# Kernel optimization log

Hardware: AMD Instinct MI355X
Metric: run time of the kernel (lower is better)

## Reference

```python
import jax, jax.numpy as jnp
import numpy as np

N = 500_000
N_ATOMS = 5
T = 8                # angle triplets per (residue, bead) table row
CONT_LEN = 36
GATE_OFFSET = 1
NUM_EXPERTS = 18
BEAD_COL = 36
MAX_BEADS = 4
ANGLE_WEIGHT = 1.0
EPS = 1e-8
MIN_LEN = 0.02


def setup_inputs() -> dict:
    key = jax.random.key(0)
    ks = jax.random.split(key, 8)
    x = jax.random.uniform(ks[0], (N, 38), dtype=jnp.float32)
    # gate column holds residue id in [1, num_experts]; bead column in [0, max_beads)
    res = jax.random.randint(ks[1], (N,), 1, NUM_EXPERTS + 1).astype(jnp.float32)
    bead = jax.random.randint(ks[2], (N,), 0, MAX_BEADS).astype(jnp.float32)
    x = x.at[:, CONT_LEN + 1].set(res)
    x = x.at[:, BEAD_COL].set(bead)
    y_true = jax.random.normal(ks[3], (N, N_ATOMS * 3), dtype=jnp.float32)
    y_pred = jax.random.normal(ks[4], (N, N_ATOMS * 3), dtype=jnp.float32)
    mask = (jax.random.uniform(ks[5], (N, N_ATOMS * 3)) < 0.85).astype(jnp.float32)
    # -1 entries act as invalid-triplet sentinels (trip_ok branch)
    trip = jax.random.randint(ks[6], (NUM_EXPERTS, MAX_BEADS, T, 3), -1, N_ATOMS, dtype=jnp.int32)
    valid = jax.random.randint(ks[7], (NUM_EXPERTS, MAX_BEADS, T), 0, 2, dtype=jnp.int32)
    return {"x": x, "y_true": y_true, "y_pred": y_pred, "mask": mask,
            "angle_triplets_table": trip, "angle_valid_table": valid}


def _atom_mse(true, pred, m):
    # masked per-atom squared error, normalized by count of valid atoms per sample
    se_atom = jnp.sum(jnp.square(true - pred) * m, axis=-1)          # [N, A]
    atom_valid = jnp.any(m > 0.0, axis=-1).astype(se_atom.dtype)     # [N, A]
    num = jnp.sum(se_atom * atom_valid, axis=-1)
    den = jnp.sum(atom_valid, axis=-1) + EPS
    return jnp.mean(num / den)


def _angle_loss(x, true, pred, m, trip_table, valid_table):
    gate = x[:, CONT_LEN + 1]
    gate = jnp.where(jnp.isfinite(gate), gate, 0.0)
    res_id = jnp.clip(jnp.round(gate).astype(jnp.int32) - GATE_OFFSET, 0, NUM_EXPERTS - 1)
    bead = x[:, BEAD_COL]
    bead = jnp.where(jnp.isfinite(bead), bead, 0.0)
    bead_id = jnp.clip(jnp.round(bead).astype(jnp.int32), 0, MAX_BEADS - 1)

    atom_valid = jnp.any(m > 0.0, axis=-1)                           # [N, A]
    trip = trip_table[res_id, bead_id]                               # [N, T, 3]
    base_valid = valid_table[res_id, bead_id]                        # [N, T]
    trip_ok = jnp.all(trip >= 0, axis=-1)
    ts = jnp.maximum(trip, 0)
    i_idx, j_idx, k_idx = ts[..., 0], ts[..., 1], ts[..., 2]         # [N, T]

    rows = jnp.arange(true.shape[0])[:, None]
    vi = atom_valid[rows, i_idx]
    vj = atom_valid[rows, j_idx]
    vk = atom_valid[rows, k_idx]
    ti, tj, tk = true[rows, i_idx], true[rows, j_idx], true[rows, k_idx]   # [N, T, 3]
    pi, pj, pk = pred[rows, i_idx], pred[rows, j_idx], pred[rows, k_idx]

    v1t, v2t, v1p, v2p = ti - tj, tk - tj, pi - pj, pk - pj
    ml2 = jnp.float32(MIN_LEN * MIN_LEN)
    sq = lambda v: jnp.sum(jnp.square(v), axis=-1)
    l1t2, l2t2, l1p2, l2p2 = sq(v1t), sq(v2t), sq(v1p), sq(v2p)

    valid = (trip_ok & (base_valid > 0) & vi & vj & vk
             & (l1t2 > ml2) & (l2t2 > ml2) & (l1p2 > ml2) & (l2p2 > ml2))

    unit = lambda v, l2: v * jax.lax.rsqrt(jnp.maximum(l2, ml2))[..., None]
    u1t, u2t = unit(v1t, l1t2), unit(v2t, l2t2)
    u1p, u2p = unit(v1p, l1p2), unit(v2p, l2p2)

    clip = lambda c: jnp.clip(c, -1.0 + 1e-6, 1.0 - 1e-6)
    cos_t = clip(jnp.sum(u1t * u2t, axis=-1))
    cos_p = clip(jnp.sum(u1p * u2p, axis=-1))
    sin_t = jnp.linalg.norm(jnp.cross(u1t, u2t), axis=-1)
    sin_p = jnp.linalg.norm(jnp.cross(u1p, u2p), axis=-1)

    per_ang = jnp.square(cos_p - cos_t) + jnp.square(sin_p - sin_t)
    per_ang = jnp.where(valid, per_ang, 0.0)
    num = jnp.sum(per_ang, axis=-1)
    den = jnp.sum(valid.astype(jnp.float32), axis=-1) + EPS
    return jnp.mean(num / den)


def reference(x, y_true, y_pred, mask, angle_triplets_table, angle_valid_table):
    true = y_true.reshape(-1, N_ATOMS, 3).astype(jnp.float32)
    pred = y_pred.reshape(-1, N_ATOMS, 3).astype(jnp.float32)
    m = mask.reshape(-1, N_ATOMS, 3).astype(jnp.float32)
    atom = _atom_mse(true, pred, m)
    ang = _angle_loss(x, true, pred, m, angle_triplets_table, angle_valid_table)
    return atom + ANGLE_WEIGHT * ang
```

## Files before the change

### kernel.cpp

```cpp
#include <hip/hip_runtime.h>
#include <math.h>

#define NATOMS 5
#define NEXP 18
#define NBEAD 4
#define EPSV 1e-8f
#define ML2 (0.02f * 0.02f)

__global__ void pack_tables(const int* __restrict__ trip, const int* __restrict__ valid,
                            int4* __restrict__ ptbl) {
    int c = blockIdx.x * blockDim.x + threadIdx.x;
    if (c < NEXP * NBEAD) {
        unsigned wv[4] = {0u, 0u, 0u, 0u};
#pragma unroll
        for (int t = 0; t < 8; t++) {
            int b = c * 8 + t;
            int i = trip[b * 3 + 0], j = trip[b * 3 + 1], k = trip[b * 3 + 2];
            int ok = (i >= 0 && j >= 0 && k >= 0 && valid[b] > 0) ? 1 : 0;
            int ic = min(max(i, 0), NATOMS - 1);
            int jc = min(max(j, 0), NATOMS - 1);
            int kc = min(max(k, 0), NATOMS - 1);
            unsigned e = (unsigned)ic | ((unsigned)jc << 3) | ((unsigned)kc << 6) |
                         ((unsigned)ok << 9);
            wv[t >> 1] |= e << ((t & 1) * 16);
        }
        ptbl[c] = make_int4((int)wv[0], (int)wv[1], (int)wv[2], (int)wv[3]);
    }
}

__device__ __forceinline__ void sel5(const float* a, int idx, float& vx, float& vy, float& vz) {
    vx = a[0]; vy = a[1]; vz = a[2];
#pragma unroll
    for (int q = 1; q < 5; q++) {
        bool c = (idx == q);
        vx = c ? a[3 * q + 0] : vx;
        vy = c ? a[3 * q + 1] : vy;
        vz = c ? a[3 * q + 2] : vz;
    }
}

__global__ __launch_bounds__(256) void loss_kernel(
    const float* __restrict__ xin, const float* __restrict__ y_true,
    const float* __restrict__ y_pred, const float* __restrict__ mask,
    const int4* __restrict__ ptbl, float* __restrict__ out, int n, float inv_n) {
    __shared__ float sT[3840];
    __shared__ float sP[3840];
    __shared__ float sM[3840];
    __shared__ float red[4];

    const int row0 = blockIdx.x * 256;
    int rows = n - row0;
    if (rows > 256) rows = 256;
    const int cnt = rows * 15;
    const int cnt4 = cnt >> 2;

    const float4* gt = reinterpret_cast<const float4*>(y_true + (size_t)row0 * 15);
    const float4* gp = reinterpret_cast<const float4*>(y_pred + (size_t)row0 * 15);
    const float4* gm = reinterpret_cast<const float4*>(mask + (size_t)row0 * 15);
    for (int i = threadIdx.x; i < cnt4; i += 256) {
        reinterpret_cast<float4*>(sT)[i] = gt[i];
        reinterpret_cast<float4*>(sP)[i] = gp[i];
        reinterpret_cast<float4*>(sM)[i] = gm[i];
    }
    for (int i = (cnt4 << 2) + threadIdx.x; i < cnt; i += 256) {
        sT[i] = y_true[(size_t)row0 * 15 + i];
        sP[i] = y_pred[(size_t)row0 * 15 + i];
        sM[i] = mask[(size_t)row0 * 15 + i];
    }
    __syncthreads();

    float result = 0.0f;
    const int row = row0 + threadIdx.x;
    if (row < n) {
        float T[15], P[15];
        const float* st = sT + threadIdx.x * 15;
        const float* sp = sP + threadIdx.x * 15;
        const float* sm = sM + threadIdx.x * 15;
#pragma unroll
        for (int c = 0; c < 15; c++) { T[c] = st[c]; P[c] = sp[c]; }

        float num_a = 0.f, den_a = 0.f;
        int avm = 0;
#pragma unroll
        for (int a = 0; a < 5; a++) {
            float se = 0.f;
            bool av = false;
#pragma unroll
            for (int c = 0; c < 3; c++) {
                float m = sm[a * 3 + c];
                float d = T[a * 3 + c] - P[a * 3 + c];
                se = fmaf(d * d, m, se);
                av = av || (m > 0.f);
            }
            if (av) { num_a += se; den_a += 1.f; avm |= (1 << a); }
        }
        result = num_a / (den_a + EPSV);

        float2 gb = *reinterpret_cast<const float2*>(xin + (size_t)row * 38 + 36);
        float bead = gb.x, gate = gb.y;
        if (!isfinite(gate)) gate = 0.f;
        if (!isfinite(bead)) bead = 0.f;
        gate = fminf(fmaxf(gate, -64.f), 64.f);
        bead = fminf(fmaxf(bead, -64.f), 64.f);
        int res_id = min(max((int)rintf(gate) - 1, 0), NEXP - 1);
        int bead_id = min(max((int)rintf(bead), 0), NBEAD - 1);

        int4 pk = ptbl[res_id * NBEAD + bead_id];
        unsigned pw0 = (unsigned)pk.x, pw1 = (unsigned)pk.y;
        unsigned pw2 = (unsigned)pk.z, pw3 = (unsigned)pk.w;

        float num_g = 0.f, den_g = 0.f;
#pragma unroll
        for (int t = 0; t < 8; t++) {
            unsigned wrd = (t < 2) ? pw0 : (t < 4) ? pw1 : (t < 6) ? pw2 : pw3;
            unsigned e = (wrd >> ((t & 1) * 16)) & 0xffffu;
            int ii = e & 7, jj = (e >> 3) & 7, kk = (e >> 6) & 7;
            bool wok = ((e >> 9) & 1u) != 0u;

            float tix, tiy, tiz, tjx, tjy, tjz, tkx, tky, tkz;
            sel5(T, ii, tix, tiy, tiz);
            sel5(T, jj, tjx, tjy, tjz);
            sel5(T, kk, tkx, tky, tkz);
            float pix, piy, piz, pjx, pjy, pjz, pkx, pky, pkz;
            sel5(P, ii, pix, piy, piz);
            sel5(P, jj, pjx, pjy, pjz);
            sel5(P, kk, pkx, pky, pkz);

            float v1tx = tix - tjx, v1ty = tiy - tjy, v1tz = tiz - tjz;
            float v2tx = tkx - tjx, v2ty = tky - tjy, v2tz = tkz - tjz;
            float v1px = pix - pjx, v1py = piy - pjy, v1pz = piz - pjz;
            float v2px = pkx - pjx, v2py = pky - pjy, v2pz = pkz - pjz;

            float l1t = v1tx * v1tx + v1ty * v1ty + v1tz * v1tz;
            float l2t = v2tx * v2tx + v2ty * v2ty + v2tz * v2tz;
            float l1p = v1px * v1px + v1py * v1py + v1pz * v1pz;
            float l2p = v2px * v2px + v2py * v2py + v2pz * v2pz;

            bool valid = wok && ((avm >> ii) & 1) && ((avm >> jj) & 1) && ((avm >> kk) & 1) &&
                         (l1t > ML2) && (l2t > ML2) && (l1p > ML2) && (l2p > ML2);

            float rt = rsqrtf(fmaxf(l1t, ML2)) * rsqrtf(fmaxf(l2t, ML2));
            float rp = rsqrtf(fmaxf(l1p, ML2)) * rsqrtf(fmaxf(l2p, ML2));

            float dott = v1tx * v2tx + v1ty * v2ty + v1tz * v2tz;
            float dotp = v1px * v2px + v1py * v2py + v1pz * v2pz;
            float cost = fminf(fmaxf(dott * rt, -1.f + 1e-6f), 1.f - 1e-6f);
            float cosp = fminf(fmaxf(dotp * rp, -1.f + 1e-6f), 1.f - 1e-6f);

            float cxt = v1ty * v2tz - v1tz * v2ty;
            float cyt = v1tz * v2tx - v1tx * v2tz;
            float czt = v1tx * v2ty - v1ty * v2tx;
            float sint = sqrtf(cxt * cxt + cyt * cyt + czt * czt) * rt;
            float cxp = v1py * v2pz - v1pz * v2py;
            float cyp = v1pz * v2px - v1px * v2pz;
            float czp = v1px * v2py - v1py * v2px;
            float sinp = sqrtf(cxp * cxp + cyp * cyp + czp * czp) * rp;

            float dc = cosp - cost, dsn = sinp - sint;
            float pa = dc * dc + dsn * dsn;
            if (valid) { num_g += pa; den_g += 1.f; }
        }
        result += num_g / (den_g + EPSV);
    }

#pragma unroll
    for (int off = 32; off > 0; off >>= 1)
        result += __shfl_down(result, off, 64);
    int lane = threadIdx.x & 63, wv = threadIdx.x >> 6;
    if (lane == 0) red[wv] = result;
    __syncthreads();
    if (threadIdx.x == 0) {
        float s = red[0] + red[1] + red[2] + red[3];
        atomicAdd(out, s * inv_n);
    }
}

extern "C" void kernel_launch(void* const* d_in, const int* in_sizes, int n_in,
                              void* d_out, int out_size, void* d_ws, size_t ws_size,
                              hipStream_t stream) {
    const float* x = (const float*)d_in[0];
    const float* y_true = (const float*)d_in[1];
    const float* y_pred = (const float*)d_in[2];
    const float* mask = (const float*)d_in[3];
    const int* trip = (const int*)d_in[4];
    const int* valid = (const int*)d_in[5];
    float* out = (float*)d_out;

    const int n = in_sizes[1] / 15;
    int4* ptbl = (int4*)d_ws;

    hipMemsetAsync(out, 0, sizeof(float), stream);
    pack_tables<<<1, 128, 0, stream>>>(trip, valid, ptbl);
    const int blocks = (n + 255) / 256;
    loss_kernel<<<blocks, 256, 0, stream>>>(x, y_true, y_pred, mask, ptbl, out, n,
                                            1.0f / (float)n);
}
```

Before: 198.1 us.

## Fuse table packing into loss kernel, bit-pack mask in LDS, simplify angle math

Drops the separate pack_tables launch: each block now rebuilds the triplet table in shared memory (three 10-bit-packed words per entry) from the global trip/valid arrays. The mask is no longer staged as floats in LDS but compressed into a 15-bit per-row bitmask through shared atomicOr, which cuts LDS footprint. That footprint cut makes the higher occupancy hint in launch_bounds(256,5) feasible. Sine is derived from the cosine as sqrt(1-c^2) instead of cross products, with one combined rsq per vector pair. The trade-offs are redundant table construction in every block, LDS atomics, and slightly different numerics for the sine term.

Result: faster. 193.9 us (-2.1%).

```diff
diff --git a/kernel.cpp b/kernel.cpp
--- a/kernel.cpp
+++ b/kernel.cpp
@@ -7,27 +7,6 @@
 #define EPSV 1e-8f
 #define ML2 (0.02f * 0.02f)
 
-__global__ void pack_tables(const int* __restrict__ trip, const int* __restrict__ valid,
-                            int4* __restrict__ ptbl) {
-    int c = blockIdx.x * blockDim.x + threadIdx.x;
-    if (c < NEXP * NBEAD) {
-        unsigned wv[4] = {0u, 0u, 0u, 0u};
-#pragma unroll
-        for (int t = 0; t < 8; t++) {
-            int b = c * 8 + t;
-            int i = trip[b * 3 + 0], j = trip[b * 3 + 1], k = trip[b * 3 + 2];
-            int ok = (i >= 0 && j >= 0 && k >= 0 && valid[b] > 0) ? 1 : 0;
-            int ic = min(max(i, 0), NATOMS - 1);
-            int jc = min(max(j, 0), NATOMS - 1);
-            int kc = min(max(k, 0), NATOMS - 1);
-            unsigned e = (unsigned)ic | ((unsigned)jc << 3) | ((unsigned)kc << 6) |
-                         ((unsigned)ok << 9);
-            wv[t >> 1] |= e << ((t & 1) * 16);
-        }
-        ptbl[c] = make_int4((int)wv[0], (int)wv[1], (int)wv[2], (int)wv[3]);
-    }
-}
-
 __device__ __forceinline__ void sel5(const float* a, int idx, float& vx, float& vy, float& vz) {
     vx = a[0]; vy = a[1]; vz = a[2];
 #pragma unroll
@@ -39,81 +18,118 @@
     }
 }
 
-__global__ __launch_bounds__(256) void loss_kernel(
+__global__ __launch_bounds__(256, 5) void loss_kernel(
     const float* __restrict__ xin, const float* __restrict__ y_true,
     const float* __restrict__ y_pred, const float* __restrict__ mask,
-    const int4* __restrict__ ptbl, float* __restrict__ out, int n, float inv_n) {
+    const int* __restrict__ trip, const int* __restrict__ valid,
+    float* __restrict__ out, int n, float inv_n) {
     __shared__ float sT[3840];
     __shared__ float sP[3840];
-    __shared__ float sM[3840];
+    __shared__ unsigned sMask[256];
+    __shared__ unsigned sTbl[72][3];
     __shared__ float red[4];
+
+    const int tid = threadIdx.x;
+
+    sMask[tid] = 0u;
+    if (tid < NEXP * NBEAD) {
+        unsigned w0 = 0u, w1 = 0u, w2 = 0u;
+#pragma unroll
+        for (int t = 0; t < 8; t++) {
+            int b = tid * 8 + t;
+            int i = trip[b * 3 + 0], j = trip[b * 3 + 1], k = trip[b * 3 + 2];
+            unsigned ok = (i >= 0 && j >= 0 && k >= 0 && valid[b] > 0) ? 1u : 0u;
+            unsigned ic = (unsigned)min(max(i, 0), NATOMS - 1);
+            unsigned jc = (unsigned)min(max(j, 0), NATOMS - 1);
+            unsigned kc = (unsigned)min(max(k, 0), NATOMS - 1);
+            unsigned e = ic | (jc << 3) | (kc << 6) | (ok << 9);
+            if (t < 3) w0 |= e << (t * 10);
+            else if (t < 6) w1 |= e << ((t - 3) * 10);
+            else w2 |= e << ((t - 6) * 10);
+        }
+        sTbl[tid][0] = w0; sTbl[tid][1] = w1; sTbl[tid][2] = w2;
+    }
+    __syncthreads();
 
     const int row0 = blockIdx.x * 256;
     int rows = n - row0;
     if (rows > 256) rows = 256;
     const int cnt = rows * 15;
     const int cnt4 = cnt >> 2;
-
-    const float4* gt = reinterpret_cast<const float4*>(y_true + (size_t)row0 * 15);
-    const float4* gp = reinterpret_cast<const float4*>(y_pred + (size_t)row0 * 15);
-    const float4* gm = reinterpret_cast<const float4*>(mask + (size_t)row0 * 15);
-    for (int i = threadIdx.x; i < cnt4; i += 256) {
-        reinterpret_cast<float4*>(sT)[i] = gt[i];
-        reinterpret_cast<float4*>(sP)[i] = gp[i];
-        reinterpret_cast<float4*>(sM)[i] = gm[i];
-    }
-    for (int i = (cnt4 << 2) + threadIdx.x; i < cnt; i += 256) {
-        sT[i] = y_true[(size_t)row0 * 15 + i];
-        sP[i] = y_pred[(size_t)row0 * 15 + i];
-        sM[i] = mask[(size_t)row0 * 15 + i];
+    const size_t base = (size_t)row0 * 15;
+
+    const float4* gt = reinterpret_cast<const float4*>(y_true + base);
+    const float4* gp = reinterpret_cast<const float4*>(y_pred + base);
+    const float4* gm = reinterpret_cast<const float4*>(mask + base);
+    for (int i = tid; i < cnt4; i += 256) {
+        float4 t4 = gt[i];
+        float4 p4 = gp[i];
+        float4 m4 = gm[i];
+        reinterpret_cast<float4*>(sT)[i] = t4;
+        reinterpret_cast<float4*>(sP)[i] = p4;
+        int e = i << 2;
+        int r = e / 15;
+        int p = e - r * 15;
+        unsigned b0 = (m4.x > 0.f ? 1u : 0u) | (m4.y > 0.f ? 2u : 0u) |
+                      (m4.z > 0.f ? 4u : 0u) | (m4.w > 0.f ? 8u : 0u);
+        unsigned sh = b0 << p;
+        unsigned lo = sh & 0x7fffu;
+        unsigned hi = sh >> 15;
+        atomicOr(&sMask[r], lo);
+        if (hi) atomicOr(&sMask[r + 1], hi);
+    }
+    for (int i = (cnt4 << 2) + tid; i < cnt; i += 256) {
+        sT[i] = y_true[base + i];
+        sP[i] = y_pred[base + i];
+        if (mask[base + i] > 0.f) {
+            int r = i / 15;
+            atomicOr(&sMask[r], 1u << (i - r * 15));
+        }
     }
     __syncthreads();
 
     float result = 0.0f;
-    const int row = row0 + threadIdx.x;
+    const int row = row0 + tid;
     if (row < n) {
         float T[15], P[15];
-        const float* st = sT + threadIdx.x * 15;
-        const float* sp = sP + threadIdx.x * 15;
-        const float* sm = sM + threadIdx.x * 15;
+        const float* st = sT + tid * 15;
+        const float* sp = sP + tid * 15;
 #pragma unroll
         for (int c = 0; c < 15; c++) { T[c] = st[c]; P[c] = sp[c]; }
+        const unsigned mrow = sMask[tid];
 
         float num_a = 0.f, den_a = 0.f;
         int avm = 0;
 #pragma unroll
         for (int a = 0; a < 5; a++) {
+            unsigned mb = (mrow >> (3 * a)) & 7u;
             float se = 0.f;
-            bool av = false;
 #pragma unroll
             for (int c = 0; c < 3; c++) {
-                float m = sm[a * 3 + c];
-                float d = T[a * 3 + c] - P[a * 3 + c];
-                se = fmaf(d * d, m, se);
-                av = av || (m > 0.f);
+                float d = T[3 * a + c] - P[3 * a + c];
+                se += ((mb >> c) & 1u) ? d * d : 0.f;
             }
-            if (av) { num_a += se; den_a += 1.f; avm |= (1 << a); }
+            if (mb) { num_a += se; den_a += 1.f; avm |= (1 << a); }
         }
         result = num_a / (den_a + EPSV);
 
         float2 gb = *reinterpret_cast<const float2*>(xin + (size_t)row * 38 + 36);
         float bead = gb.x, gate = gb.y;
-        if (!isfinite(gate)) gate = 0.f;
-        if (!isfinite(bead)) bead = 0.f;
-        gate = fminf(fmaxf(gate, -64.f), 64.f);
-        bead = fminf(fmaxf(bead, -64.f), 64.f);
+        gate = isfinite(gate) ? gate : 0.f;
+        bead = isfinite(bead) ? bead : 0.f;
+        gate = fminf(fmaxf(gate, -1e6f), 1e6f);
+        bead = fminf(fmaxf(bead, -1e6f), 1e6f);
         int res_id = min(max((int)rintf(gate) - 1, 0), NEXP - 1);
         int bead_id = min(max((int)rintf(bead), 0), NBEAD - 1);
-
-        int4 pk = ptbl[res_id * NBEAD + bead_id];
-        unsigned pw0 = (unsigned)pk.x, pw1 = (unsigned)pk.y;
-        unsigned pw2 = (unsigned)pk.z, pw3 = (unsigned)pk.w;
+        int combo = res_id * NBEAD + bead_id;
+        unsigned w0 = sTbl[combo][0], w1 = sTbl[combo][1], w2 = sTbl[combo][2];
 
         float num_g = 0.f, den_g = 0.f;
 #pragma unroll
         for (int t = 0; t < 8; t++) {
-            unsigned wrd = (t < 2) ? pw0 : (t < 4) ? pw1 : (t < 6) ? pw2 : pw3;
-            unsigned e = (wrd >> ((t & 1) * 16)) & 0xffffu;
+            unsigned wrd = (t < 3) ? w0 : (t < 6) ? w1 : w2;
+            int sh = (t < 3) ? t : (t < 6) ? (t - 3) : (t - 6);
+            unsigned e = (wrd >> (sh * 10)) & 0x3ffu;
             int ii = e & 7, jj = (e >> 3) & 7, kk = (e >> 6) & 7;
             bool wok = ((e >> 9) & 1u) != 0u;
 
@@ -131,34 +147,30 @@
             float v1px = pix - pjx, v1py = piy - pjy, v1pz = piz - pjz;
             float v2px = pkx - pjx, v2py = pky - pjy, v2pz = pkz - pjz;
 
-            float l1t = v1tx * v1tx + v1ty * v1ty + v1tz * v1tz;
-            float l2t = v2tx * v2tx + v2ty * v2ty + v2tz * v2tz;
-            float l1p = v1px * v1px + v1py * v1py + v1pz * v1pz;
-            float l2p = v2px * v2px + v2py * v2py + v2pz * v2pz;
+            float l1t = fmaf(v1tx, v1tx, fmaf(v1ty, v1ty, v1tz * v1tz));
+            float l2t = fmaf(v2tx, v2tx, fmaf(v2ty, v2ty, v2tz * v2tz));
+            float l1p = fmaf(v1px, v1px, fmaf(v1py, v1py, v1pz * v1pz));
+            float l2p = fmaf(v2px, v2px, fmaf(v2py, v2py, v2pz * v2pz));
 
             bool valid = wok && ((avm >> ii) & 1) && ((avm >> jj) & 1) && ((avm >> kk) & 1) &&
                          (l1t > ML2) && (l2t > ML2) && (l1p > ML2) && (l2p > ML2);
 
-            float rt = rsqrtf(fmaxf(l1t, ML2)) * rsqrtf(fmaxf(l2t, ML2));
-            float rp = rsqrtf(fmaxf(l1p, ML2)) * rsqrtf(fmaxf(l2p, ML2));
-
-            float dott = v1tx * v2tx + v1ty * v2ty + v1tz * v2tz;
-            float dotp = v1px * v2px + v1py * v2py + v1pz * v2pz;
-            float cost = fminf(fmaxf(dott * rt, -1.f + 1e-6f), 1.f - 1e-6f);
-            float cosp = fminf(fmaxf(dotp * rp, -1.f + 1e-6f), 1.f - 1e-6f);
-
-            float cxt = v1ty * v2tz - v1tz * v2ty;
-            float cyt = v1tz * v2tx - v1tx * v2tz;
-            float czt = v1tx * v2ty - v1ty * v2tx;
-            float sint = sqrtf(cxt * cxt + cyt * cyt + czt * czt) * rt;
-            float cxp = v1py * v2pz - v1pz * v2py;
-            float cyp = v1pz * v2px - v1px * v2pz;
-            float czp = v1px * v2py - v1py * v2px;
-            float sinp = sqrtf(cxp * cxp + cyp * cyp + czp * czp) * rp;
+            float rt = __builtin_amdgcn_rsqf(fmaxf(l1t, ML2) * fmaxf(l2t, ML2));
+            float rp = __builtin_amdgcn_rsqf(fmaxf(l1p, ML2) * fmaxf(l2p, ML2));
+
+            float dott = fmaf(v1tx, v2tx, fmaf(v1ty, v2ty, v1tz * v2tz));
+            float dotp = fmaf(v1px, v2px, fmaf(v1py, v2py, v1pz * v2pz));
+            float cut = dott * rt;
+            float cup = dotp * rp;
+            float cost = fminf(fmaxf(cut, -1.f + 1e-6f), 1.f - 1e-6f);
+            float cosp = fminf(fmaxf(cup, -1.f + 1e-6f), 1.f - 1e-6f);
+            float s2t = fmaxf(fmaf(-cut, cut, 1.f), 0.f);
+            float s2p = fmaxf(fmaf(-cup, cup, 1.f), 0.f);
+            float sint = __builtin_amdgcn_sqrtf(s2t);
+            float sinp = __builtin_amdgcn_sqrtf(s2p);
 
             float dc = cosp - cost, dsn = sinp - sint;
-            float pa = dc * dc + dsn * dsn;
-            if (valid) { num_g += pa; den_g += 1.f; }
+            if (valid) { num_g += fmaf(dc, dc, dsn * dsn); den_g += 1.f; }
         }
         result += num_g / (den_g + EPSV);
     }
@@ -166,10 +178,10 @@
 #pragma unroll
     for (int off = 32; off > 0; off >>= 1)
         result += __shfl_down(result, off, 64);
-    int lane = threadIdx.x & 63, wv = threadIdx.x >> 6;
+    int lane = tid & 63, wv = tid >> 6;
     if (lane == 0) red[wv] = result;
     __syncthreads();
-    if (threadIdx.x == 0) {
+    if (tid == 0) {
         float s = red[0] + red[1] + red[2] + red[3];
         atomicAdd(out, s * inv_n);
     }
@@ -187,11 +199,9 @@
     float* out = (float*)d_out;
 
     const int n = in_sizes[1] / 15;
-    int4* ptbl = (int4*)d_ws;
 
     hipMemsetAsync(out, 0, sizeof(float), stream);
-    pack_tables<<<1, 128, 0, stream>>>(trip, valid, ptbl);
     const int blocks = (n + 255) / 256;
-    loss_kernel<<<blocks, 256, 0, stream>>>(x, y_true, y_pred, mask, ptbl, out, n,
+    loss_kernel<<<blocks, 256, 0, stream>>>(x, y_true, y_pred, mask, trip, valid, out, n,
                                             1.0f / (float)n);
 }
```
